# Optimization experiments

Hardware: AMD Instinct MI355X
Metric: run time of the kernel (lower is better)

## Reference

```python
import jax, jax.numpy as jnp
import numpy as np

N_NODES = 50000
NEG_SLOPE = 0.2  # PyG GATConv default LeakyReLU slope


def gat_conv(x, src, dst, W, att_src, att_dst, bias, heads, out_ch, concat):
    """PyG-style GATConv (dropout=0, add_self_loops omitted to match raw edge list usage).
    x: [N, in], W: [in, heads*out_ch], att_*: [1, heads, out_ch], bias: [heads*out_ch] or [out_ch].
    Messages flow src -> dst; softmax normalizes over incoming edges of each dst node."""
    N = x.shape[0]
    h = (x @ W).reshape(N, heads, out_ch)                      # [N,H,C]
    a_s = (h * att_src).sum(-1)                                # [N,H]
    a_d = (h * att_dst).sum(-1)                                # [N,H]
    e = jax.nn.leaky_relu(a_s[src] + a_d[dst], NEG_SLOPE)      # [E,H] per-edge logits
    m = jax.ops.segment_max(e, dst, num_segments=N)            # [N,H] stable softmax max
    p = jnp.exp(e - m[dst])                                    # [E,H]
    s = jax.ops.segment_sum(p, dst, num_segments=N)            # [N,H]
    alpha = p / (s[dst] + 1e-16)                               # [E,H] attention coeffs
    out = jax.ops.segment_sum(h[src] * alpha[:, :, None], dst, num_segments=N)  # [N,H,C]
    out = out.reshape(N, heads * out_ch) if concat else out.mean(axis=1)
    return out + bias


def setup_inputs() -> dict:
    key = jax.random.key(0)
    ks = jax.random.split(key, 10)
    in_ch, hid, heads, out_ch = 128, 32, 4, 64
    E = 800000
    x = jax.random.normal(ks[0], (N_NODES, in_ch), dtype=jnp.float32)
    edge_index = jax.random.randint(ks[1], (2, E), 0, N_NODES, dtype=jnp.int64)
    sc = 0.1
    return {
        "x": x,
        "edge_index": edge_index,
        "W1": jax.random.normal(ks[2], (in_ch, heads * hid), dtype=jnp.float32) * sc,
        "att_src1": jax.random.normal(ks[3], (1, heads, hid), dtype=jnp.float32) * sc,
        "att_dst1": jax.random.normal(ks[4], (1, heads, hid), dtype=jnp.float32) * sc,
        "b1": jnp.zeros((heads * hid,), dtype=jnp.float32),
        "W2": jax.random.normal(ks[5], (heads * hid, out_ch), dtype=jnp.float32) * sc,
        "att_src2": jax.random.normal(ks[6], (1, 1, out_ch), dtype=jnp.float32) * sc,
        "att_dst2": jax.random.normal(ks[7], (1, 1, out_ch), dtype=jnp.float32) * sc,
        "b2": jnp.zeros((out_ch,), dtype=jnp.float32),
    }


def reference(x, edge_index, W1, att_src1, att_dst1, b1, W2, att_src2, att_dst2, b2):
    src, dst = edge_index[0], edge_index[1]
    h = gat_conv(x, src, dst, W1, att_src1, att_dst1, b1, heads=4, out_ch=32, concat=True)
    h = jax.nn.elu(h)
    out = gat_conv(h, src, dst, W2, att_src2, att_dst2, b2, heads=1, out_ch=64, concat=False)
    return out
```

## Files before the change

kernel.cpp:

```cpp
#include <hip/hip_runtime.h>

#define N_NODES 50000
#define N_EDGES 800000
#define GEMM_BLKS ((N_NODES + 63) / 64)
#define NGRP 8
#define RANGE ((N_NODES + NGRP - 1) / NGRP)
#define FILL_BLKS 4096
#define EDGES_PER_BLK 1564
#define MAXDEG 64
#define AGG_BLKS (N_NODES / 4)

typedef __attribute__((ext_vector_type(8))) short bf16x8;
typedef __attribute__((ext_vector_type(4))) float f32x4;
typedef unsigned short u16;
typedef unsigned int u32;

__device__ __forceinline__ float lrelu(float x) { return x > 0.f ? x : 0.2f * x; }

__device__ __forceinline__ u16 f2bf(float f) {
    u32 u = __float_as_uint(f);
    return (u16)((u + 0x7FFFu + ((u >> 16) & 1u)) >> 16);
}
__device__ __forceinline__ float bflo(u32 w) { return __uint_as_float(w << 16); }
__device__ __forceinline__ float bfhi(u32 w) { return __uint_as_float(w & 0xFFFF0000u); }
__device__ __forceinline__ float elu(float x) { return x > 0.f ? x : __expf(x) - 1.f; }

__global__ __launch_bounds__(256) void k_fill(
    const int* __restrict__ src, const int* __restrict__ dst,
    int* __restrict__ deg, int* __restrict__ col)
{
    const int g = blockIdx.x & 7;
    const int b = blockIdx.x >> 3;
    const int lo = g * RANGE;
    const int hi = min(lo + RANGE, N_NODES);
    const int e0 = b * EDGES_PER_BLK;
    const int e1 = min(e0 + EDGES_PER_BLK, N_EDGES);
    for (int e = e0 + threadIdx.x; e < e1; e += 256) {
        int v = dst[e];
        if (v >= lo && v < hi) {
            int pos = atomicAdd(&deg[v], 1);
            if (pos < MAXDEG) col[v * MAXDEG + pos] = src[e];
        }
    }
}

__global__ __launch_bounds__(256) void k_prep(
    const float* __restrict__ W1, const float* __restrict__ as1v, const float* __restrict__ ad1v,
    const float* __restrict__ W2, const float* __restrict__ as2v, const float* __restrict__ ad2v,
    u16* __restrict__ Wt1, u16* __restrict__ Wt2)
{
    int gid = blockIdx.x * 256 + threadIdx.x;
    if (gid < 144 * 128) {
        int n = gid >> 7, k = gid & 127;
        float v = 0.f;
        if (n < 128) v = W1[k * 128 + n];
        else if (n < 136) {
            int h = n - 128;
            const float* att = (h < 4) ? as1v : ad1v;
            int hh = h & 3;
            float s = 0.f;
            for (int c = 0; c < 32; ++c) s += W1[k * 128 + hh * 32 + c] * att[hh * 32 + c];
            v = s;
        }
        Wt1[n * 128 + k] = f2bf(v);
    } else {
        int g2 = gid - 144 * 128;
        if (g2 < 80 * 128) {
            int n = g2 >> 7, k = g2 & 127;
            float v = 0.f;
            if (n < 64) v = W2[k * 64 + n];
            else if (n == 64) { float s = 0.f; for (int c = 0; c < 64; ++c) s += W2[k * 64 + c] * as2v[c]; v = s; }
            else if (n == 65) { float s = 0.f; for (int c = 0; c < 64; ++c) s += W2[k * 64 + c] * ad2v[c]; v = s; }
            Wt2[n * 128 + k] = f2bf(v);
        }
    }
}

__global__ __launch_bounds__(256) void k_gemm1(
    const float* __restrict__ x, const u16* __restrict__ Wt1,
    u16* __restrict__ hbf, float* __restrict__ as_, float* __restrict__ ad_)
{
    __shared__ u16 xs[64][136];
    __shared__ u16 ws[144][136];
    const int t = threadIdx.x;
    const int n0 = blockIdx.x * 64;
    #pragma unroll
    for (int it = 0; it < 8; ++it) {
        int idx = it * 256 + t;
        int row = idx >> 5, c4 = (idx & 31) * 4;
        int n = n0 + row;
        float4 xv = make_float4(0.f, 0.f, 0.f, 0.f);
        if (n < N_NODES) xv = *(const float4*)&x[(size_t)n * 128 + c4];
        uint2 pk;
        pk.x = (u32)f2bf(xv.x) | ((u32)f2bf(xv.y) << 16);
        pk.y = (u32)f2bf(xv.z) | ((u32)f2bf(xv.w) << 16);
        *(uint2*)&xs[row][c4] = pk;
    }
    #pragma unroll
    for (int it = 0; it < 9; ++it) {
        int idx = it * 256 + t;
        int row = idx >> 4, c8 = (idx & 15) * 8;
        *(uint4*)&ws[row][c8] = *(const uint4*)&Wt1[row * 128 + c8];
    }
    __syncthreads();
    const int l = t & 63, w = t >> 6;
    const int lm = l & 15, quad = l >> 4;
    f32x4 acc[9];
    #pragma unroll
    for (int nt = 0; nt < 9; ++nt) acc[nt] = (f32x4){0.f, 0.f, 0.f, 0.f};
    const u16* arow = &xs[w * 16 + lm][0];
    #pragma unroll
    for (int kc = 0; kc < 4; ++kc) {
        int k0 = kc * 32 + quad * 8;
        bf16x8 a = *(const bf16x8*)&arow[k0];
        #pragma unroll
        for (int nt = 0; nt < 9; ++nt) {
            bf16x8 b = *(const bf16x8*)&ws[nt * 16 + lm][k0];
            acc[nt] = __builtin_amdgcn_mfma_f32_16x16x32_bf16(a, b, acc[nt], 0, 0, 0);
        }
    }
    #pragma unroll
    for (int r = 0; r < 4; ++r) {
        int n = n0 + w * 16 + quad * 4 + r;
        if (n >= N_NODES) continue;
        #pragma unroll
        for (int nt = 0; nt < 8; ++nt)
            hbf[(size_t)n * 128 + nt * 16 + lm] = f2bf(acc[nt][r]);
        if (lm < 4)      as_[n * 4 + lm]     = acc[8][r];
        else if (lm < 8) ad_[n * 4 + lm - 4] = acc[8][r];
    }
}

__global__ __launch_bounds__(256) void k_agg1(
    const int* __restrict__ deg, const int* __restrict__ col,
    const float* __restrict__ as_, const float* __restrict__ ad_,
    const u32* __restrict__ h1u, const float* __restrict__ b1,
    u32* __restrict__ out1u)
{
    const int t = threadIdx.x;
    const int wv = t >> 6;
    const int l = t & 63;
    const int v = blockIdx.x * 4 + wv;
    const int c = l & 15;
    const int slot = l >> 4;
    const int hh = c >> 2;
    const int dg = min(deg[v], MAXDEG);
    const float adh = ad_[v * 4 + hh];
    const int base = v * MAXDEG;
    float a[8] = {0.f, 0.f, 0.f, 0.f, 0.f, 0.f, 0.f, 0.f};
    float s = 0.f;
    for (int i0 = slot; i0 < dg; i0 += 8) {
        int i1 = i0 + 4;
        bool m1 = i1 < dg;
        int u0 = col[base + i0];
        int u1 = col[base + (m1 ? i1 : i0)];
        float p0 = __expf(lrelu(as_[u0 * 4 + hh] + adh));
        float p1 = m1 ? __expf(lrelu(as_[u1 * 4 + hh] + adh)) : 0.f;
        uint4 w0 = *(const uint4*)(h1u + (u0 << 6) + (c << 2));
        uint4 w1 = *(const uint4*)(h1u + (u1 << 6) + (c << 2));
        a[0] = fmaf(p0, bflo(w0.x), a[0]); a[1] = fmaf(p0, bfhi(w0.x), a[1]);
        a[2] = fmaf(p0, bflo(w0.y), a[2]); a[3] = fmaf(p0, bfhi(w0.y), a[3]);
        a[4] = fmaf(p0, bflo(w0.z), a[4]); a[5] = fmaf(p0, bfhi(w0.z), a[5]);
        a[6] = fmaf(p0, bflo(w0.w), a[6]); a[7] = fmaf(p0, bfhi(w0.w), a[7]);
        a[0] = fmaf(p1, bflo(w1.x), a[0]); a[1] = fmaf(p1, bfhi(w1.x), a[1]);
        a[2] = fmaf(p1, bflo(w1.y), a[2]); a[3] = fmaf(p1, bfhi(w1.y), a[3]);
        a[4] = fmaf(p1, bflo(w1.z), a[4]); a[5] = fmaf(p1, bfhi(w1.z), a[5]);
        a[6] = fmaf(p1, bflo(w1.w), a[6]); a[7] = fmaf(p1, bfhi(w1.w), a[7]);
        s += p0 + p1;
    }
    #pragma unroll
    for (int k = 0; k < 8; ++k) {
        a[k] += __shfl_xor(a[k], 16);
        a[k] += __shfl_xor(a[k], 32);
    }
    s += __shfl_xor(s, 16);
    s += __shfl_xor(s, 32);
    if (slot == 0) {
        float inv = 1.f / (s + 1e-16f);
        float4 b0 = *(const float4*)&b1[8 * c];
        float4 b4 = *(const float4*)&b1[8 * c + 4];
        float o0 = elu(a[0] * inv + b0.x);
        float o1 = elu(a[1] * inv + b0.y);
        float o2 = elu(a[2] * inv + b0.z);
        float o3 = elu(a[3] * inv + b0.w);
        float o4 = elu(a[4] * inv + b4.x);
        float o5 = elu(a[5] * inv + b4.y);
        float o6 = elu(a[6] * inv + b4.z);
        float o7 = elu(a[7] * inv + b4.w);
        uint4 pk;
        pk.x = (u32)f2bf(o0) | ((u32)f2bf(o1) << 16);
        pk.y = (u32)f2bf(o2) | ((u32)f2bf(o3) << 16);
        pk.z = (u32)f2bf(o4) | ((u32)f2bf(o5) << 16);
        pk.w = (u32)f2bf(o6) | ((u32)f2bf(o7) << 16);
        *(uint4*)(out1u + v * 64 + 4 * c) = pk;
    }
}

__global__ __launch_bounds__(256) void k_gemm2(
    const u16* __restrict__ xbf, const u16* __restrict__ Wt2,
    u16* __restrict__ hbf, float* __restrict__ as_, float* __restrict__ ad_)
{
    __shared__ u16 xs[64][136];
    __shared__ u16 ws[80][136];
    const int t = threadIdx.x;
    const int n0 = blockIdx.x * 64;
    #pragma unroll
    for (int it = 0; it < 4; ++it) {
        int idx = it * 256 + t;
        int row = idx >> 4, c8 = (idx & 15) * 8;
        int n = n0 + row;
        uint4 vv = make_uint4(0u, 0u, 0u, 0u);
        if (n < N_NODES) vv = *(const uint4*)&xbf[(size_t)n * 128 + c8];
        *(uint4*)&xs[row][c8] = vv;
    }
    #pragma unroll
    for (int it = 0; it < 5; ++it) {
        int idx = it * 256 + t;
        int row = idx >> 4, c8 = (idx & 15) * 8;
        *(uint4*)&ws[row][c8] = *(const uint4*)&Wt2[row * 128 + c8];
    }
    __syncthreads();
    const int l = t & 63, w = t >> 6;
    const int lm = l & 15, quad = l >> 4;
    f32x4 acc[5];
    #pragma unroll
    for (int nt = 0; nt < 5; ++nt) acc[nt] = (f32x4){0.f, 0.f, 0.f, 0.f};
    const u16* arow = &xs[w * 16 + lm][0];
    #pragma unroll
    for (int kc = 0; kc < 4; ++kc) {
        int k0 = kc * 32 + quad * 8;
        bf16x8 a = *(const bf16x8*)&arow[k0];
        #pragma unroll
        for (int nt = 0; nt < 5; ++nt) {
            bf16x8 b = *(const bf16x8*)&ws[nt * 16 + lm][k0];
            acc[nt] = __builtin_amdgcn_mfma_f32_16x16x32_bf16(a, b, acc[nt], 0, 0, 0);
        }
    }
    #pragma unroll
    for (int r = 0; r < 4; ++r) {
        int n = n0 + w * 16 + quad * 4 + r;
        if (n >= N_NODES) continue;
        #pragma unroll
        for (int nt = 0; nt < 4; ++nt)
            hbf[(size_t)n * 64 + nt * 16 + lm] = f2bf(acc[nt][r]);
        if (lm == 0)      as_[n] = acc[4][r];
        else if (lm == 1) ad_[n] = acc[4][r];
    }
}

__global__ __launch_bounds__(256) void k_agg2(
    const int* __restrict__ deg, const int* __restrict__ col,
    const float* __restrict__ as_, const float* __restrict__ ad_,
    const u32* __restrict__ h2u, const float* __restrict__ b2,
    float* __restrict__ out)
{
    const int t = threadIdx.x;
    const int wv = t >> 6;
    const int l = t & 63;
    const int v = blockIdx.x * 4 + wv;
    const int c = l & 7;
    const int slot = l >> 3;
    const int dg = min(deg[v], MAXDEG);
    const float adh = ad_[v];
    const int base = v * MAXDEG;
    float a[8] = {0.f, 0.f, 0.f, 0.f, 0.f, 0.f, 0.f, 0.f};
    float s = 0.f;
    for (int i0 = slot; i0 < dg; i0 += 16) {
        int i1 = i0 + 8;
        bool m1 = i1 < dg;
        int u0 = col[base + i0];
        int u1 = col[base + (m1 ? i1 : i0)];
        float p0 = __expf(lrelu(as_[u0] + adh));
        float p1 = m1 ? __expf(lrelu(as_[u1] + adh)) : 0.f;
        uint4 w0 = *(const uint4*)(h2u + (u0 << 5) + (c << 2));
        uint4 w1 = *(const uint4*)(h2u + (u1 << 5) + (c << 2));
        a[0] = fmaf(p0, bflo(w0.x), a[0]); a[1] = fmaf(p0, bfhi(w0.x), a[1]);
        a[2] = fmaf(p0, bflo(w0.y), a[2]); a[3] = fmaf(p0, bfhi(w0.y), a[3]);
        a[4] = fmaf(p0, bflo(w0.z), a[4]); a[5] = fmaf(p0, bfhi(w0.z), a[5]);
        a[6] = fmaf(p0, bflo(w0.w), a[6]); a[7] = fmaf(p0, bfhi(w0.w), a[7]);
        a[0] = fmaf(p1, bflo(w1.x), a[0]); a[1] = fmaf(p1, bfhi(w1.x), a[1]);
        a[2] = fmaf(p1, bflo(w1.y), a[2]); a[3] = fmaf(p1, bfhi(w1.y), a[3]);
        a[4] = fmaf(p1, bflo(w1.z), a[4]); a[5] = fmaf(p1, bfhi(w1.z), a[5]);
        a[6] = fmaf(p1, bflo(w1.w), a[6]); a[7] = fmaf(p1, bfhi(w1.w), a[7]);
        s += p0 + p1;
    }
    #pragma unroll
    for (int k = 0; k < 8; ++k) {
        a[k] += __shfl_xor(a[k], 8);
        a[k] += __shfl_xor(a[k], 16);
        a[k] += __shfl_xor(a[k], 32);
    }
    s += __shfl_xor(s, 8);
    s += __shfl_xor(s, 16);
    s += __shfl_xor(s, 32);
    if (slot == 0) {
        float inv = 1.f / (s + 1e-16f);
        float4 b0 = *(const float4*)&b2[8 * c];
        float4 b4 = *(const float4*)&b2[8 * c + 4];
        float4 oa, ob;
        oa.x = a[0] * inv + b0.x;
        oa.y = a[1] * inv + b0.y;
        oa.z = a[2] * inv + b0.z;
        oa.w = a[3] * inv + b0.w;
        ob.x = a[4] * inv + b4.x;
        ob.y = a[5] * inv + b4.y;
        ob.z = a[6] * inv + b4.z;
        ob.w = a[7] * inv + b4.w;
        *(float4*)&out[(size_t)v * 64 + 8 * c]     = oa;
        *(float4*)&out[(size_t)v * 64 + 8 * c + 4] = ob;
    }
}

extern "C" void kernel_launch(void* const* d_in, const int* in_sizes, int n_in,
                              void* d_out, int out_size, void* d_ws, size_t ws_size,
                              hipStream_t stream)
{
    const float* x      = (const float*)d_in[0];
    const int*   ei     = (const int*)d_in[1];
    const float* W1     = (const float*)d_in[2];
    const float* att_s1 = (const float*)d_in[3];
    const float* att_d1 = (const float*)d_in[4];
    const float* b1     = (const float*)d_in[5];
    const float* W2     = (const float*)d_in[6];
    const float* att_s2 = (const float*)d_in[7];
    const float* att_d2 = (const float*)d_in[8];
    const float* b2     = (const float*)d_in[9];
    const int* src = ei;
    const int* dst = ei + N_EDGES;
    float* out = (float*)d_out;

    char* wsp = (char*)d_ws;
    u16* Wt1   = (u16*)wsp;  wsp += 144 * 128 * 2;
    u16* Wt2   = (u16*)wsp;  wsp += 80 * 128 * 2;
    u16* h1bf  = (u16*)wsp;  wsp += (size_t)N_NODES * 128 * 2;
    u16* o1bf  = (u16*)wsp;  wsp += (size_t)N_NODES * 128 * 2;
    u16* h2bf  = (u16*)wsp;  wsp += (size_t)N_NODES * 64 * 2;
    float* as1 = (float*)wsp; wsp += (size_t)N_NODES * 4 * 4;
    float* ad1 = (float*)wsp; wsp += (size_t)N_NODES * 4 * 4;
    float* as2 = (float*)wsp; wsp += (size_t)N_NODES * 4;
    float* ad2 = (float*)wsp; wsp += (size_t)N_NODES * 4;
    int* deg   = (int*)wsp;   wsp += (size_t)N_NODES * 4;
    int* col   = (int*)wsp;   wsp += (size_t)N_NODES * MAXDEG * 4;

    k_prep<<<112, 256, 0, stream>>>(W1, att_s1, att_d1, W2, att_s2, att_d2, Wt1, Wt2);
    hipMemsetAsync(deg, 0, (size_t)N_NODES * 4, stream);
    k_fill<<<FILL_BLKS, 256, 0, stream>>>(src, dst, deg, col);

    k_gemm1<<<GEMM_BLKS, 256, 0, stream>>>(x, Wt1, h1bf, as1, ad1);
    k_agg1<<<AGG_BLKS, 256, 0, stream>>>(deg, col, as1, ad1, (const u32*)h1bf, b1, (u32*)o1bf);

    k_gemm2<<<GEMM_BLKS, 256, 0, stream>>>(o1bf, Wt2, h2bf, as2, ad2);
    k_agg2<<<AGG_BLKS, 256, 0, stream>>>(deg, col, as2, ad2, (const u32*)h2bf, b2, out);
}
```

Measured before the change: 208.7 us.

## Fuse CSR fill into GEMM1 launch, head-major h1 layout, 16-bit column indices

```diff
diff --git a/kernel.cpp b/kernel.cpp
--- a/kernel.cpp
+++ b/kernel.cpp
@@ -3,12 +3,13 @@
 #define N_NODES 50000
 #define N_EDGES 800000
 #define GEMM_BLKS ((N_NODES + 63) / 64)
-#define NGRP 8
-#define RANGE ((N_NODES + NGRP - 1) / NGRP)
 #define FILL_BLKS 4096
+#define FRONT_BLKS (GEMM_BLKS + FILL_BLKS)
+#define RANGE 6250
 #define EDGES_PER_BLK 1564
 #define MAXDEG 64
-#define AGG_BLKS (N_NODES / 4)
+#define AGG1_BLKS (4 * (N_NODES / 8))
+#define AGG2_BLKS (N_NODES / 4)
 
 typedef __attribute__((ext_vector_type(8))) short bf16x8;
 typedef __attribute__((ext_vector_type(4))) float f32x4;
@@ -24,25 +25,6 @@
 __device__ __forceinline__ float bflo(u32 w) { return __uint_as_float(w << 16); }
 __device__ __forceinline__ float bfhi(u32 w) { return __uint_as_float(w & 0xFFFF0000u); }
 __device__ __forceinline__ float elu(float x) { return x > 0.f ? x : __expf(x) - 1.f; }
-
-__global__ __launch_bounds__(256) void k_fill(
-    const int* __restrict__ src, const int* __restrict__ dst,
-    int* __restrict__ deg, int* __restrict__ col)
-{
-    const int g = blockIdx.x & 7;
-    const int b = blockIdx.x >> 3;
-    const int lo = g * RANGE;
-    const int hi = min(lo + RANGE, N_NODES);
-    const int e0 = b * EDGES_PER_BLK;
-    const int e1 = min(e0 + EDGES_PER_BLK, N_EDGES);
-    for (int e = e0 + threadIdx.x; e < e1; e += 256) {
-        int v = dst[e];
-        if (v >= lo && v < hi) {
-            int pos = atomicAdd(&deg[v], 1);
-            if (pos < MAXDEG) col[v * MAXDEG + pos] = src[e];
-        }
-    }
-}
 
 __global__ __launch_bounds__(256) void k_prep(
     const float* __restrict__ W1, const float* __restrict__ as1v, const float* __restrict__ ad1v,
@@ -76,13 +58,32 @@
     }
 }
 
-__global__ __launch_bounds__(256) void k_gemm1(
+__global__ __launch_bounds__(256) void k_front(
     const float* __restrict__ x, const u16* __restrict__ Wt1,
-    u16* __restrict__ hbf, float* __restrict__ as_, float* __restrict__ ad_)
+    u16* __restrict__ h1t, float* __restrict__ as_, float* __restrict__ ad_,
+    const int* __restrict__ src, const int* __restrict__ dst,
+    int* __restrict__ deg, u16* __restrict__ col16)
 {
     __shared__ u16 xs[64][136];
     __shared__ u16 ws[144][136];
     const int t = threadIdx.x;
+    if (blockIdx.x >= GEMM_BLKS) {
+        const int bb = blockIdx.x - GEMM_BLKS;
+        const int g = bb & 7;
+        const int b = bb >> 3;
+        const int lo = g * RANGE;
+        const int hi = min(lo + RANGE, N_NODES);
+        const int e0 = b * EDGES_PER_BLK;
+        const int e1 = min(e0 + EDGES_PER_BLK, N_EDGES);
+        for (int e = e0 + t; e < e1; e += 256) {
+            int v = dst[e];
+            if (v >= lo && v < hi) {
+                int pos = atomicAdd(&deg[v], 1);
+                if (pos < MAXDEG) col16[v * MAXDEG + pos] = (u16)src[e];
+            }
+        }
+        return;
+    }
     const int n0 = blockIdx.x * 64;
     #pragma unroll
     for (int it = 0; it < 8; ++it) {
@@ -125,74 +126,55 @@
         if (n >= N_NODES) continue;
         #pragma unroll
         for (int nt = 0; nt < 8; ++nt)
-            hbf[(size_t)n * 128 + nt * 16 + lm] = f2bf(acc[nt][r]);
+            h1t[(size_t)(nt >> 1) * N_NODES * 32 + (size_t)n * 32 + (nt & 1) * 16 + lm]
+                = f2bf(acc[nt][r]);
         if (lm < 4)      as_[n * 4 + lm]     = acc[8][r];
         else if (lm < 8) ad_[n * 4 + lm - 4] = acc[8][r];
     }
 }
 
 __global__ __launch_bounds__(256) void k_agg1(
-    const int* __restrict__ deg, const int* __restrict__ col,
+    const int* __restrict__ deg, const u16* __restrict__ col16,
     const float* __restrict__ as_, const float* __restrict__ ad_,
-    const u32* __restrict__ h1u, const float* __restrict__ b1,
+    const u32* __restrict__ h1t, const float* __restrict__ b1,
     u32* __restrict__ out1u)
 {
+    const int g = blockIdx.x & 3;
+    const int nb = blockIdx.x >> 2;
     const int t = threadIdx.x;
-    const int wv = t >> 6;
-    const int l = t & 63;
-    const int v = blockIdx.x * 4 + wv;
+    const int w = t >> 6, l = t & 63;
+    const int sub = l >> 5;
+    const int slot = (l >> 4) & 1;
     const int c = l & 15;
-    const int slot = l >> 4;
-    const int hh = c >> 2;
+    const int v = nb * 8 + w * 2 + sub;
     const int dg = min(deg[v], MAXDEG);
-    const float adh = ad_[v * 4 + hh];
-    const int base = v * MAXDEG;
-    float a[8] = {0.f, 0.f, 0.f, 0.f, 0.f, 0.f, 0.f, 0.f};
-    float s = 0.f;
-    for (int i0 = slot; i0 < dg; i0 += 8) {
-        int i1 = i0 + 4;
+    const float adh = ad_[v * 4 + g];
+    const u32* hg = h1t + (size_t)g * N_NODES * 16;
+    const u16* cr = col16 + v * MAXDEG;
+    float a0 = 0.f, a1 = 0.f, s = 0.f;
+    for (int i0 = slot; i0 < dg; i0 += 4) {
+        int i1 = i0 + 2;
         bool m1 = i1 < dg;
-        int u0 = col[base + i0];
-        int u1 = col[base + (m1 ? i1 : i0)];
-        float p0 = __expf(lrelu(as_[u0 * 4 + hh] + adh));
-        float p1 = m1 ? __expf(lrelu(as_[u1 * 4 + hh] + adh)) : 0.f;
-        uint4 w0 = *(const uint4*)(h1u + (u0 << 6) + (c << 2));
-        uint4 w1 = *(const uint4*)(h1u + (u1 << 6) + (c << 2));
-        a[0] = fmaf(p0, bflo(w0.x), a[0]); a[1] = fmaf(p0, bfhi(w0.x), a[1]);
-        a[2] = fmaf(p0, bflo(w0.y), a[2]); a[3] = fmaf(p0, bfhi(w0.y), a[3]);
-        a[4] = fmaf(p0, bflo(w0.z), a[4]); a[5] = fmaf(p0, bfhi(w0.z), a[5]);
-        a[6] = fmaf(p0, bflo(w0.w), a[6]); a[7] = fmaf(p0, bfhi(w0.w), a[7]);
-        a[0] = fmaf(p1, bflo(w1.x), a[0]); a[1] = fmaf(p1, bfhi(w1.x), a[1]);
-        a[2] = fmaf(p1, bflo(w1.y), a[2]); a[3] = fmaf(p1, bfhi(w1.y), a[3]);
-        a[4] = fmaf(p1, bflo(w1.z), a[4]); a[5] = fmaf(p1, bfhi(w1.z), a[5]);
-        a[6] = fmaf(p1, bflo(w1.w), a[6]); a[7] = fmaf(p1, bfhi(w1.w), a[7]);
+        int u0 = __builtin_nontemporal_load(&cr[i0]);
+        int u1 = __builtin_nontemporal_load(&cr[m1 ? i1 : i0]);
+        float p0 = __expf(lrelu(as_[u0 * 4 + g] + adh));
+        float p1 = m1 ? __expf(lrelu(as_[u1 * 4 + g] + adh)) : 0.f;
+        u32 w0 = hg[u0 * 16 + c];
+        u32 w1 = hg[u1 * 16 + c];
+        a0 = fmaf(p0, bflo(w0), a0); a1 = fmaf(p0, bfhi(w0), a1);
+        a0 = fmaf(p1, bflo(w1), a0); a1 = fmaf(p1, bfhi(w1), a1);
         s += p0 + p1;
     }
-    #pragma unroll
-    for (int k = 0; k < 8; ++k) {
-        a[k] += __shfl_xor(a[k], 16);
-        a[k] += __shfl_xor(a[k], 32);
-    }
-    s += __shfl_xor(s, 16);
-    s += __shfl_xor(s, 32);
+    a0 += __shfl_xor(a0, 16);
+    a1 += __shfl_xor(a1, 16);
+    s  += __shfl_xor(s, 16);
     if (slot == 0) {
         float inv = 1.f / (s + 1e-16f);
-        float4 b0 = *(const float4*)&b1[8 * c];
-        float4 b4 = *(const float4*)&b1[8 * c + 4];
-        float o0 = elu(a[0] * inv + b0.x);
-        float o1 = elu(a[1] * inv + b0.y);
-        float o2 = elu(a[2] * inv + b0.z);
-        float o3 = elu(a[3] * inv + b0.w);
-        float o4 = elu(a[4] * inv + b4.x);
-        float o5 = elu(a[5] * inv + b4.y);
-        float o6 = elu(a[6] * inv + b4.z);
-        float o7 = elu(a[7] * inv + b4.w);
-        uint4 pk;
-        pk.x = (u32)f2bf(o0) | ((u32)f2bf(o1) << 16);
-        pk.y = (u32)f2bf(o2) | ((u32)f2bf(o3) << 16);
-        pk.z = (u32)f2bf(o4) | ((u32)f2bf(o5) << 16);
-        pk.w = (u32)f2bf(o6) | ((u32)f2bf(o7) << 16);
-        *(uint4*)(out1u + v * 64 + 4 * c) = pk;
+        int ch = g * 32 + 2 * c;
+        float o0 = elu(a0 * inv + b1[ch]);
+        float o1 = elu(a1 * inv + b1[ch + 1]);
+        u32 pk = (u32)f2bf(o0) | ((u32)f2bf(o1) << 16);
+        __builtin_nontemporal_store(pk, &out1u[(size_t)v * 64 + g * 16 + c]);
     }
 }
 
@@ -249,7 +231,7 @@
 }
 
 __global__ __launch_bounds__(256) void k_agg2(
-    const int* __restrict__ deg, const int* __restrict__ col,
+    const int* __restrict__ deg, const u16* __restrict__ col16,
     const float* __restrict__ as_, const float* __restrict__ ad_,
     const u32* __restrict__ h2u, const float* __restrict__ b2,
     float* __restrict__ out)
@@ -262,14 +244,14 @@
     const int slot = l >> 3;
     const int dg = min(deg[v], MAXDEG);
     const float adh = ad_[v];
-    const int base = v * MAXDEG;
+    const u16* cr = col16 + v * MAXDEG;
     float a[8] = {0.f, 0.f, 0.f, 0.f, 0.f, 0.f, 0.f, 0.f};
     float s = 0.f;
     for (int i0 = slot; i0 < dg; i0 += 16) {
         int i1 = i0 + 8;
         bool m1 = i1 < dg;
-        int u0 = col[base + i0];
-        int u1 = col[base + (m1 ? i1 : i0)];
+        int u0 = __builtin_nontemporal_load(&cr[i0]);
+        int u1 = __builtin_nontemporal_load(&cr[m1 ? i1 : i0]);
         float p0 = __expf(lrelu(as_[u0] + adh));
         float p1 = m1 ? __expf(lrelu(as_[u1] + adh)) : 0.f;
         uint4 w0 = *(const uint4*)(h2u + (u0 << 5) + (c << 2));
@@ -332,7 +314,7 @@
     char* wsp = (char*)d_ws;
     u16* Wt1   = (u16*)wsp;  wsp += 144 * 128 * 2;
     u16* Wt2   = (u16*)wsp;  wsp += 80 * 128 * 2;
-    u16* h1bf  = (u16*)wsp;  wsp += (size_t)N_NODES * 128 * 2;
+    u16* h1t   = (u16*)wsp;  wsp += (size_t)N_NODES * 128 * 2;
     u16* o1bf  = (u16*)wsp;  wsp += (size_t)N_NODES * 128 * 2;
     u16* h2bf  = (u16*)wsp;  wsp += (size_t)N_NODES * 64 * 2;
     float* as1 = (float*)wsp; wsp += (size_t)N_NODES * 4 * 4;
@@ -340,15 +322,12 @@
     float* as2 = (float*)wsp; wsp += (size_t)N_NODES * 4;
     float* ad2 = (float*)wsp; wsp += (size_t)N_NODES * 4;
     int* deg   = (int*)wsp;   wsp += (size_t)N_NODES * 4;
-    int* col   = (int*)wsp;   wsp += (size_t)N_NODES * MAXDEG * 4;
+    u16* col16 = (u16*)wsp;  wsp += (size_t)N_NODES * MAXDEG * 2;
 
     k_prep<<<112, 256, 0, stream>>>(W1, att_s1, att_d1, W2, att_s2, att_d2, Wt1, Wt2);
     hipMemsetAsync(deg, 0, (size_t)N_NODES * 4, stream);
-    k_fill<<<FILL_BLKS, 256, 0, stream>>>(src, dst, deg, col);
-
-    k_gemm1<<<GEMM_BLKS, 256, 0, stream>>>(x, Wt1, h1bf, as1, ad1);
-    k_agg1<<<AGG_BLKS, 256, 0, stream>>>(deg, col, as1, ad1, (const u32*)h1bf, b1, (u32*)o1bf);
-
+    k_front<<<FRONT_BLKS, 256, 0, stream>>>(x, Wt1, h1t, as1, ad1, src, dst, deg, col16);
+    k_agg1<<<AGG1_BLKS, 256, 0, stream>>>(deg, col16, as1, ad1, (const u32*)h1t, b1, (u32*)o1bf);
     k_gemm2<<<GEMM_BLKS, 256, 0, stream>>>(o1bf, Wt2, h2bf, as2, ad2);
-    k_agg2<<<AGG_BLKS, 256, 0, stream>>>(deg, col, as2, ad2, (const u32*)h2bf, b2, out);
-}
+    k_agg2<<<AGG2_BLKS, 256, 0, stream>>>(deg, col16, as2, ad2, (const u32*)h2bf, b2, out);
+}
```

After: 294.6 us. 1.41x slower.
